# Kernel tuning notes

Hardware: AMD Instinct MI355X
Metric: run time of the kernel (lower is better)

Reference implementation:

```python
import jax, jax.numpy as jnp
import numpy as np

N = 40000
E = 640000
IN_CH = 256
HEADS = 4
C = 32  # hidden_channels per head
NEG_SLOPE = 0.2  # PyG GATConv default


def setup_inputs() -> dict:
    key = jax.random.key(0)
    k1, k2, k3, k4, k5, k6 = jax.random.split(key, 6)
    x = jax.random.normal(k1, (N, IN_CH), dtype=jnp.float32)
    edge_index = jax.random.randint(k2, (2, E), 0, N, dtype=jnp.int64)
    batch = jnp.zeros((N,), dtype=jnp.int64)
    # GATConv params (glorot-ish scale)
    W = jax.random.normal(k3, (IN_CH, HEADS * C), dtype=jnp.float32) / np.sqrt(IN_CH)
    att_src = jax.random.normal(k4, (HEADS, C), dtype=jnp.float32) / np.sqrt(C)
    att_dst = jax.random.normal(k5, (HEADS, C), dtype=jnp.float32) / np.sqrt(C)
    bias = jnp.zeros((HEADS * C,), dtype=jnp.float32)
    return {"x": x, "edge_index": edge_index, "batch": batch,
            "W": W, "att_src": att_src, "att_dst": att_dst, "bias": bias}


def _gat_forward(x, src, dst, W, att_src, att_dst, bias):
    n = x.shape[0]
    xp = (x @ W).reshape(n, HEADS, C)                      # [N,H,C]
    a_src = jnp.einsum('nhc,hc->nh', xp, att_src)          # [N,H]
    a_dst = jnp.einsum('nhc,hc->nh', xp, att_dst)          # [N,H]
    e = a_src[src] + a_dst[dst]                            # [E',H]
    e = jnp.where(e > 0, e, NEG_SLOPE * e)                 # LeakyReLU
    # segment softmax over edges grouped by destination node
    e_max = jax.ops.segment_max(e, dst, num_segments=n)    # [N,H]
    e_exp = jnp.exp(e - e_max[dst])                        # [E',H]
    e_sum = jax.ops.segment_sum(e_exp, dst, num_segments=n)
    alpha = e_exp / e_sum[dst]                             # [E',H]
    # (attention dropout p=0.6 is identity in eval mode)
    msgs = alpha[:, :, None] * xp[src]                     # [E',H,C]
    out = jax.ops.segment_sum(msgs, dst, num_segments=n)   # [N,H,C]
    out = out.reshape(n, HEADS * C) + bias                 # concat heads
    return jax.nn.relu(out)


def reference(x, edge_index, batch, W, att_src, att_dst, bias):
    n = x.shape[0]
    loops = jnp.arange(n, dtype=edge_index.dtype)
    src = jnp.concatenate([edge_index[0], loops])          # add self-loops (PyG default)
    dst = jnp.concatenate([edge_index[1], loops])
    return _gat_forward(x, src, dst, W, att_src, att_dst, bias)
```

## Files before the change

### kernel.cpp

```cpp
#include <hip/hip_runtime.h>
#include <hip/hip_bf16.h>
#include <stdint.h>

#define IN_CH 256
#define HC    128
#define HEADS 4
#define CPH   32
#define NEG_SLOPE 0.2f

#define NB3    625
#define BCAP3  1408
#define EPB    4096

using f32x4  = __attribute__((ext_vector_type(4))) float;
using bf16x8 = __attribute__((ext_vector_type(8))) short;
using f16x8  = __attribute__((ext_vector_type(8))) _Float16;

__global__ __launch_bounds__(256) void k_prep(const float* __restrict__ W,
                                              unsigned short* __restrict__ wpk,
                                              int* __restrict__ bcur) {
    const int t = threadIdx.x, s = blockIdx.x;
    if (s == 0) for (int i = t; i < NB3; i += 256) bcur[i] = 0;
    __shared__ float Wl[32][128];
#pragma unroll
    for (int j = 0; j < 4; ++j) {
        int idx4 = t + j * 256;
        int kk = idx4 >> 5, c4 = (idx4 & 31) * 4;
        *(float4*)(&Wl[kk][c4]) = *(const float4*)(W + (size_t)(s * 32 + kk) * HC + c4);
    }
    __syncthreads();
#pragma unroll
    for (int j = 0; j < 4; ++j) {
        int o = t + j * 256;
        int lane = o & 63, hilo = (o >> 6) & 1, ct = o >> 7;
        const int kk0 = (lane >> 4) * 8;
        const int col = ct * 16 + (lane & 15);
        unsigned short tmp[8];
#pragma unroll
        for (int e = 0; e < 8; ++e) {
            float f = Wl[kk0 + e][col];
            unsigned int u = __float_as_uint(f);
            if (hilo == 0) {
                tmp[e] = (unsigned short)(u >> 16);
            } else {
                float fl = f - __uint_as_float(u & 0xFFFF0000u);
                tmp[e] = (unsigned short)(__float_as_uint(fl) >> 16);
            }
        }
        uint4 ov;
        ov.x = tmp[0] | ((unsigned int)tmp[1] << 16);
        ov.y = tmp[2] | ((unsigned int)tmp[3] << 16);
        ov.z = tmp[4] | ((unsigned int)tmp[5] << 16);
        ov.w = tmp[6] | ((unsigned int)tmp[7] << 16);
        ((uint4*)wpk)[s * 1024 + o] = ov;
    }
}

__device__ inline void cvt_hilo(const float4& a, const float4& b, bf16x8& hi, bf16x8& lo) {
    const float f[8] = {a.x, a.y, a.z, a.w, b.x, b.y, b.z, b.w};
#pragma unroll
    for (int e = 0; e < 8; ++e) {
        unsigned int u = __float_as_uint(f[e]);
        hi[e] = (short)(u >> 16);
        float fl = f[e] - __uint_as_float(u & 0xFFFF0000u);
        lo[e] = (short)(__float_as_uint(fl) >> 16);
    }
}

__global__ __launch_bounds__(256) void k_work(const float* __restrict__ x,
                                              const unsigned short* __restrict__ wpk,
                                              const float* __restrict__ att_src,
                                              const float* __restrict__ att_dst,
                                              unsigned short* __restrict__ xp,
                                              float* __restrict__ asrc,
                                              float* __restrict__ adst,
                                              const int* __restrict__ ei,
                                              int* __restrict__ bcur,
                                              unsigned int* __restrict__ ebuf,
                                              int E, int n, int nbin) {
    if (blockIdx.x < (unsigned)nbin) {
        __shared__ int hist[NB3], base[NB3];
        const int t = threadIdx.x;
        const int e0 = blockIdx.x * EPB;
        const int EN = E + n;
        for (int i = t; i < NB3; i += 256) hist[i] = 0;
        __syncthreads();

        unsigned int pk[16];
        int rk[16];
#pragma unroll
        for (int j = 0; j < 16; ++j) {
            int e = e0 + j * 256 + t;
            if (e < EN) {
                int s, d;
                if (e < E) { s = ei[e]; d = ei[E + e]; } else { s = d = e - E; }
                pk[j] = ((unsigned int)d << 16) | (unsigned int)s;
                rk[j] = atomicAdd(&hist[d >> 6], 1);
            } else {
                pk[j] = 0xFFFFFFFFu;
                rk[j] = 0;
            }
        }
        __syncthreads();
        for (int i = t; i < NB3; i += 256) {
            int c = hist[i];
            base[i] = c ? atomicAdd(&bcur[i], c) : 0;
        }
        __syncthreads();
#pragma unroll
        for (int j = 0; j < 16; ++j) {
            if (pk[j] != 0xFFFFFFFFu) {
                int b = pk[j] >> 22;
                int pos = base[b] + rk[j];
                if (pos < BCAP3)
                    ebuf[(size_t)b * BCAP3 + pos] = pk[j];
            }
        }
        return;
    }

    const int wv = (blockIdx.x - nbin) * 4 + (threadIdx.x >> 6);
    const int m0 = (wv >> 1) * 16;
    const int h2 = wv & 1;
    if (m0 >= n) return;
    const int l  = threadIdx.x & 63;
    const int lr = l & 15;
    const int q  = l >> 4;
    const int kq = q * 8;

    f32x4 acc[4];
    const f32x4 zero = {0.f, 0.f, 0.f, 0.f};
#pragma unroll
    for (int j = 0; j < 4; ++j) acc[j] = zero;

    const int arow_idx = (m0 + lr < n) ? (m0 + lr) : (n - 1);
    const float* arow = x + (size_t)arow_idx * IN_CH + kq;
    const uint4* wb = (const uint4*)wpk + l;
    const int ctb = h2 * 4;

    float4 aLb[2], aHb[2];
    aLb[0] = *(const float4*)(arow);
    aHb[0] = *(const float4*)(arow + 4);

    uint4 sbh[2][2], sbl[2][2];
#pragma unroll
    for (int j = 0; j < 2; ++j) {
        sbh[0][j] = wb[((ctb + j) * 2 + 0) * 64];
        sbl[0][j] = wb[((ctb + j) * 2 + 1) * 64];
    }

#pragma unroll
    for (int s = 0; s < 8; ++s) {
        const int kc = s * 32;
        const int p = s & 1, pn = p ^ 1;
#pragma unroll
        for (int j = 0; j < 2; ++j) {
            sbh[1][j] = wb[((s * 8 + ctb + 2 + j) * 2 + 0) * 64];
            sbl[1][j] = wb[((s * 8 + ctb + 2 + j) * 2 + 1) * 64];
        }
        bf16x8 ahi, alo;
        cvt_hilo(aLb[p], aHb[p], ahi, alo);
#pragma unroll
        for (int j = 0; j < 2; ++j) {
            bf16x8 bhi = __builtin_bit_cast(bf16x8, sbh[0][j]);
            bf16x8 blo = __builtin_bit_cast(bf16x8, sbl[0][j]);
            acc[j] = __builtin_amdgcn_mfma_f32_16x16x32_bf16(alo, bhi, acc[j], 0, 0, 0);
            acc[j] = __builtin_amdgcn_mfma_f32_16x16x32_bf16(ahi, blo, acc[j], 0, 0, 0);
            acc[j] = __builtin_amdgcn_mfma_f32_16x16x32_bf16(ahi, bhi, acc[j], 0, 0, 0);
        }
        if (s < 7) {
#pragma unroll
            for (int j = 0; j < 2; ++j) {
                sbh[0][j] = wb[(((s + 1) * 8 + ctb + j) * 2 + 0) * 64];
                sbl[0][j] = wb[(((s + 1) * 8 + ctb + j) * 2 + 1) * 64];
            }
            aLb[pn] = *(const float4*)(arow + kc + 32);
            aHb[pn] = *(const float4*)(arow + kc + 36);
        }
#pragma unroll
        for (int j = 0; j < 2; ++j) {
            bf16x8 bhi = __builtin_bit_cast(bf16x8, sbh[1][j]);
            bf16x8 blo = __builtin_bit_cast(bf16x8, sbl[1][j]);
            acc[2 + j] = __builtin_amdgcn_mfma_f32_16x16x32_bf16(alo, bhi, acc[2 + j], 0, 0, 0);
            acc[2 + j] = __builtin_amdgcn_mfma_f32_16x16x32_bf16(ahi, blo, acc[2 + j], 0, 0, 0);
            acc[2 + j] = __builtin_amdgcn_mfma_f32_16x16x32_bf16(ahi, bhi, acc[2 + j], 0, 0, 0);
        }
    }

    float as_c[4], ad_c[4];
#pragma unroll
    for (int j = 0; j < 4; ++j) {
        as_c[j] = att_src[(ctb + j) * 16 + lr];
        ad_c[j] = att_dst[(ctb + j) * 16 + lr];
    }
#pragma unroll
    for (int hp = 0; hp < 2; ++hp)
#pragma unroll
        for (int r = 0; r < 4; ++r) {
            float s = acc[2 * hp][r] * as_c[2 * hp] + acc[2 * hp + 1][r] * as_c[2 * hp + 1];
            float d = acc[2 * hp][r] * ad_c[2 * hp] + acc[2 * hp + 1][r] * ad_c[2 * hp + 1];
            s += __shfl_xor(s, 1, 64); s += __shfl_xor(s, 2, 64);
            s += __shfl_xor(s, 4, 64); s += __shfl_xor(s, 8, 64);
            d += __shfl_xor(d, 1, 64); d += __shfl_xor(d, 2, 64);
            d += __shfl_xor(d, 4, 64); d += __shfl_xor(d, 8, 64);
            if (lr == 0) {
                int row = m0 + q * 4 + r;
                if (row < n) {
                    asrc[(size_t)row * 4 + h2 * 2 + hp] = s;
                    adst[(size_t)row * 4 + h2 * 2 + hp] = d;
                }
            }
        }

#pragma unroll
    for (int r = 0; r < 4; ++r) {
        int row = m0 + q * 4 + r;
        if (row < n) {
            unsigned short* xr = xp + (size_t)row * HC + h2 * 64 + lr;
#pragma unroll
            for (int j = 0; j < 4; ++j) {
                _Float16 hv = (_Float16)acc[j][r];
                xr[j * 16] = __builtin_bit_cast(unsigned short, hv);
            }
        }
    }
}

__global__ __launch_bounds__(512) void k_fgat(const int* __restrict__ bcur,
                                              const unsigned int* __restrict__ ebuf,
                                              const float* __restrict__ asrc,
                                              const float* __restrict__ adst,
                                              const unsigned short* __restrict__ xp,
                                              const float* __restrict__ bias,
                                              float* __restrict__ out, int n) {
    __shared__ unsigned short sL[BCAP3];
    __shared__ int lcnt[64];
    __shared__ int loff[65];
    const int b = blockIdx.x, t = threadIdx.x;
    const int m = min(bcur[b], BCAP3);
    const unsigned int* eb = ebuf + (size_t)b * BCAP3;

    unsigned int pk[3];
#pragma unroll
    for (int j = 0; j < 3; ++j) {
        int i = t + j * 512;
        pk[j] = (i < m) ? eb[i] : 0xFFFFFFFFu;
    }
    if (t < 64) lcnt[t] = 0;
    __syncthreads();
    int rk[3];
#pragma unroll
    for (int j = 0; j < 3; ++j)
        if (pk[j] != 0xFFFFFFFFu)
            rk[j] = atomicAdd(&lcnt[(pk[j] >> 16) & 63], 1);
    __syncthreads();
    if (t < 64) {
        int v = lcnt[t];
        int sum = v;
#pragma unroll
        for (int off = 1; off < 64; off <<= 1) {
            int u = __shfl_up(sum, off, 64);
            if (t >= off) sum += u;
        }
        loff[t] = sum - v;
        if (t == 63) loff[64] = sum;
    }
    __syncthreads();
#pragma unroll
    for (int j = 0; j < 3; ++j)
        if (pk[j] != 0xFFFFFFFFu) {
            int ln = (pk[j] >> 16) & 63;
            sL[loff[ln] + rk[j]] = (unsigned short)(pk[j] & 0xFFFFu);
        }
    __syncthreads();

    const int lane = t & 63;
    const int cl = lane & 15;
    const int eg = lane >> 4;
    const int hh = cl >> 2;
    const float4* bp = (const float4*)bias + cl * 2;
    const float4 b0 = bp[0], b1 = bp[1];

#pragma unroll
    for (int i8 = 0; i8 < 8; ++i8) {
        const int ln = (t >> 6) * 8 + i8;
        const int nd = b * 64 + ln;
        if (nd >= n) continue;
        const int s0 = loff[ln], e0 = loff[ln + 1];
        const float ad2 = adst[(size_t)nd * 4 + hh];

        float4 a0 = make_float4(0.f, 0.f, 0.f, 0.f);
        float4 a1 = make_float4(0.f, 0.f, 0.f, 0.f);
        float Z = 0.f;

        int i = s0;
        for (; i + 8 <= e0; i += 8) {
            int sa = sL[i + eg];
            int sb = sL[i + 4 + eg];
            float ta = asrc[(size_t)sa * 4 + hh] + ad2;
            float tb = asrc[(size_t)sb * 4 + hh] + ad2;
            uint4 ua = *(const uint4*)(xp + (size_t)sa * HC + cl * 8);
            uint4 ub = *(const uint4*)(xp + (size_t)sb * HC + cl * 8);
            f16x8 va = __builtin_bit_cast(f16x8, ua);
            f16x8 vb = __builtin_bit_cast(f16x8, ub);
            ta = ta > 0.f ? ta : NEG_SLOPE * ta;
            tb = tb > 0.f ? tb : NEG_SLOPE * tb;
            float pa = __expf(ta);
            float pb = __expf(tb);
            Z += pa + pb;
            a0.x += pa * (float)va[0]; a0.y += pa * (float)va[1];
            a0.z += pa * (float)va[2]; a0.w += pa * (float)va[3];
            a1.x += pa * (float)va[4]; a1.y += pa * (float)va[5];
            a1.z += pa * (float)va[6]; a1.w += pa * (float)va[7];
            a0.x += pb * (float)vb[0]; a0.y += pb * (float)vb[1];
            a0.z += pb * (float)vb[2]; a0.w += pb * (float)vb[3];
            a1.x += pb * (float)vb[4]; a1.y += pb * (float)vb[5];
            a1.z += pb * (float)vb[6]; a1.w += pb * (float)vb[7];
        }
        for (; i < e0; i += 4) {
            if (i + eg < e0) {
                int s = sL[i + eg];
                float tt = asrc[(size_t)s * 4 + hh] + ad2;
                uint4 u = *(const uint4*)(xp + (size_t)s * HC + cl * 8);
                f16x8 v = __builtin_bit_cast(f16x8, u);
                tt = tt > 0.f ? tt : NEG_SLOPE * tt;
                float p = __expf(tt);
                Z += p;
                a0.x += p * (float)v[0]; a0.y += p * (float)v[1];
                a0.z += p * (float)v[2]; a0.w += p * (float)v[3];
                a1.x += p * (float)v[4]; a1.y += p * (float)v[5];
                a1.z += p * (float)v[6]; a1.w += p * (float)v[7];
            }
        }

#pragma unroll
        for (int off = 16; off < 64; off <<= 1) {
            a0.x += __shfl_xor(a0.x, off, 64); a0.y += __shfl_xor(a0.y, off, 64);
            a0.z += __shfl_xor(a0.z, off, 64); a0.w += __shfl_xor(a0.w, off, 64);
            a1.x += __shfl_xor(a1.x, off, 64); a1.y += __shfl_xor(a1.y, off, 64);
            a1.z += __shfl_xor(a1.z, off, 64); a1.w += __shfl_xor(a1.w, off, 64);
            Z += __shfl_xor(Z, off, 64);
        }

        if (eg == 0) {
            const float rZ = 1.0f / Z;
            float4 o0, o1;
            o0.x = fmaxf(a0.x * rZ + b0.x, 0.f); o0.y = fmaxf(a0.y * rZ + b0.y, 0.f);
            o0.z = fmaxf(a0.z * rZ + b0.z, 0.f); o0.w = fmaxf(a0.w * rZ + b0.w, 0.f);
            o1.x = fmaxf(a1.x * rZ + b1.x, 0.f); o1.y = fmaxf(a1.y * rZ + b1.y, 0.f);
            o1.z = fmaxf(a1.z * rZ + b1.z, 0.f); o1.w = fmaxf(a1.w * rZ + b1.w, 0.f);
            float4* op = (float4*)(out + (size_t)nd * HC) + cl * 2;
            op[0] = o0; op[1] = o1;
        }
    }
}

extern "C" void kernel_launch(void* const* d_in, const int* in_sizes, int n_in,
                              void* d_out, int out_size, void* d_ws, size_t ws_size,
                              hipStream_t stream) {
    const float* x       = (const float*)d_in[0];
    const int*   ei      = (const int*)d_in[1];
    const float* W       = (const float*)d_in[3];
    const float* att_src = (const float*)d_in[4];
    const float* att_dst = (const float*)d_in[5];
    const float* bias    = (const float*)d_in[6];
    float* out = (float*)d_out;

    const int n = in_sizes[0] / IN_CH;
    const int E = in_sizes[1] / 2;
    const int EN = E + n;
    const int nbin = (EN + EPB - 1) / EPB;
    const int ngemm = (((n + 15) / 16) * 2 + 3) / 4;
    const int nbkt = (n + 63) / 64;

    unsigned short* xp = (unsigned short*)d_ws;
    float* asrc = (float*)(xp + (size_t)n * HC);
    float* adst = asrc + (size_t)n * HEADS;
    int*   bcur  = (int*)(adst + (size_t)n * HEADS);
    unsigned int* ebuf = (unsigned int*)(bcur + NB3);
    unsigned short* wpk = (unsigned short*)(((uintptr_t)(ebuf + (size_t)NB3 * BCAP3) + 63) & ~(uintptr_t)63);

    k_prep<<<8, 256, 0, stream>>>(W, wpk, bcur);
    k_work<<<nbin + ngemm, 256, 0, stream>>>(x, wpk, att_src, att_dst,
                                             xp, asrc, adst, ei, bcur, ebuf,
                                             E, n, nbin);
    k_fgat<<<nbkt, 512, 0, stream>>>(bcur, ebuf, asrc, adst, xp, bias, out, n);
}
```

Before: 71.32 us.

## Stage 16-row x tile in LDS and split GEMM heads across four waves

The GEMM part of k_work now uses one block per 16-row tile. The block cooperatively loads the x rows into padded shared memory, and each of its four waves computes one head (32 columns). Before, each wave handled two heads and read its x rows straight from global memory, so the same x data was read twice by separate waves. The change removes that duplicate global read and lowers per-wave register use, at the cost of a block barrier, LDS traffic, and twice as many GEMM blocks. It also drops the A-operand double-buffering, so global-load latency is now exposed at the tile load.

```diff
diff --git a/kernel.cpp b/kernel.cpp
--- a/kernel.cpp
+++ b/kernel.cpp
@@ -11,6 +11,7 @@
 #define NB3    625
 #define BCAP3  1408
 #define EPB    4096
+#define ALDP   260
 
 using f32x4  = __attribute__((ext_vector_type(4))) float;
 using bf16x8 = __attribute__((ext_vector_type(8))) short;
@@ -78,8 +79,11 @@
                                               int* __restrict__ bcur,
                                               unsigned int* __restrict__ ebuf,
                                               int E, int n, int nbin) {
+    __shared__ __align__(16) char smem[16 * ALDP * 4];
+
     if (blockIdx.x < (unsigned)nbin) {
-        __shared__ int hist[NB3], base[NB3];
+        int* hist = (int*)smem;
+        int* base = hist + NB3;
         const int t = threadIdx.x;
         const int e0 = blockIdx.x * EPB;
         const int EN = E + n;
@@ -119,109 +123,97 @@
         return;
     }
 
-    const int wv = (blockIdx.x - nbin) * 4 + (threadIdx.x >> 6);
-    const int m0 = (wv >> 1) * 16;
-    const int h2 = wv & 1;
+    const int bg = blockIdx.x - nbin;
+    const int m0 = bg * 16;
     if (m0 >= n) return;
-    const int l  = threadIdx.x & 63;
-    const int lr = l & 15;
-    const int q  = l >> 4;
-    const int kq = q * 8;
-
-    f32x4 acc[4];
+    const int tid = threadIdx.x;
+    const int wvl = tid >> 6;
+    const int l   = tid & 63;
+    const int lr  = l & 15;
+    const int q   = l >> 4;
+    const int kq  = q * 8;
+
+    float (*xls)[ALDP] = (float(*)[ALDP])smem;
+    {
+        const float* xb = x + (size_t)m0 * IN_CH;
+#pragma unroll
+        for (int j = 0; j < 4; ++j) {
+            int idx = tid + j * 256;
+            int row = idx >> 6, k4 = (idx & 63) * 4;
+            float4 v = *(const float4*)(xb + (size_t)row * IN_CH + k4);
+            *(float4*)(&xls[row][k4]) = v;
+        }
+    }
+    __syncthreads();
+
+    f32x4 acc[2];
     const f32x4 zero = {0.f, 0.f, 0.f, 0.f};
-#pragma unroll
-    for (int j = 0; j < 4; ++j) acc[j] = zero;
-
-    const int arow_idx = (m0 + lr < n) ? (m0 + lr) : (n - 1);
-    const float* arow = x + (size_t)arow_idx * IN_CH + kq;
+    acc[0] = zero; acc[1] = zero;
+
     const uint4* wb = (const uint4*)wpk + l;
-    const int ctb = h2 * 4;
-
-    float4 aLb[2], aHb[2];
-    aLb[0] = *(const float4*)(arow);
-    aHb[0] = *(const float4*)(arow + 4);
-
-    uint4 sbh[2][2], sbl[2][2];
-#pragma unroll
-    for (int j = 0; j < 2; ++j) {
-        sbh[0][j] = wb[((ctb + j) * 2 + 0) * 64];
-        sbl[0][j] = wb[((ctb + j) * 2 + 1) * 64];
-    }
+    const int ctb = wvl * 2;
+
+    uint4 bh0 = wb[((ctb + 0) * 2 + 0) * 64];
+    uint4 bl0 = wb[((ctb + 0) * 2 + 1) * 64];
+    uint4 bh1 = wb[((ctb + 1) * 2 + 0) * 64];
+    uint4 bl1 = wb[((ctb + 1) * 2 + 1) * 64];
 
 #pragma unroll
     for (int s = 0; s < 8; ++s) {
-        const int kc = s * 32;
-        const int p = s & 1, pn = p ^ 1;
-#pragma unroll
-        for (int j = 0; j < 2; ++j) {
-            sbh[1][j] = wb[((s * 8 + ctb + 2 + j) * 2 + 0) * 64];
-            sbl[1][j] = wb[((s * 8 + ctb + 2 + j) * 2 + 1) * 64];
-        }
+        uint4 nh0, nl0, nh1, nl1;
+        if (s < 7) {
+            nh0 = wb[(((s + 1) * 8 + ctb + 0) * 2 + 0) * 64];
+            nl0 = wb[(((s + 1) * 8 + ctb + 0) * 2 + 1) * 64];
+            nh1 = wb[(((s + 1) * 8 + ctb + 1) * 2 + 0) * 64];
+            nl1 = wb[(((s + 1) * 8 + ctb + 1) * 2 + 1) * 64];
+        }
+        float4 aL = *(const float4*)(&xls[lr][s * 32 + kq]);
+        float4 aH = *(const float4*)(&xls[lr][s * 32 + kq + 4]);
         bf16x8 ahi, alo;
-        cvt_hilo(aLb[p], aHb[p], ahi, alo);
-#pragma unroll
-        for (int j = 0; j < 2; ++j) {
-            bf16x8 bhi = __builtin_bit_cast(bf16x8, sbh[0][j]);
-            bf16x8 blo = __builtin_bit_cast(bf16x8, sbl[0][j]);
-            acc[j] = __builtin_amdgcn_mfma_f32_16x16x32_bf16(alo, bhi, acc[j], 0, 0, 0);
-            acc[j] = __builtin_amdgcn_mfma_f32_16x16x32_bf16(ahi, blo, acc[j], 0, 0, 0);
-            acc[j] = __builtin_amdgcn_mfma_f32_16x16x32_bf16(ahi, bhi, acc[j], 0, 0, 0);
-        }
-        if (s < 7) {
-#pragma unroll
-            for (int j = 0; j < 2; ++j) {
-                sbh[0][j] = wb[(((s + 1) * 8 + ctb + j) * 2 + 0) * 64];
-                sbl[0][j] = wb[(((s + 1) * 8 + ctb + j) * 2 + 1) * 64];
-            }
-            aLb[pn] = *(const float4*)(arow + kc + 32);
-            aHb[pn] = *(const float4*)(arow + kc + 36);
-        }
-#pragma unroll
-        for (int j = 0; j < 2; ++j) {
-            bf16x8 bhi = __builtin_bit_cast(bf16x8, sbh[1][j]);
-            bf16x8 blo = __builtin_bit_cast(bf16x8, sbl[1][j]);
-            acc[2 + j] = __builtin_amdgcn_mfma_f32_16x16x32_bf16(alo, bhi, acc[2 + j], 0, 0, 0);
-            acc[2 + j] = __builtin_amdgcn_mfma_f32_16x16x32_bf16(ahi, blo, acc[2 + j], 0, 0, 0);
-            acc[2 + j] = __builtin_amdgcn_mfma_f32_16x16x32_bf16(ahi, bhi, acc[2 + j], 0, 0, 0);
-        }
-    }
-
-    float as_c[4], ad_c[4];
-#pragma unroll
-    for (int j = 0; j < 4; ++j) {
-        as_c[j] = att_src[(ctb + j) * 16 + lr];
-        ad_c[j] = att_dst[(ctb + j) * 16 + lr];
-    }
-#pragma unroll
-    for (int hp = 0; hp < 2; ++hp)
-#pragma unroll
-        for (int r = 0; r < 4; ++r) {
-            float s = acc[2 * hp][r] * as_c[2 * hp] + acc[2 * hp + 1][r] * as_c[2 * hp + 1];
-            float d = acc[2 * hp][r] * ad_c[2 * hp] + acc[2 * hp + 1][r] * ad_c[2 * hp + 1];
-            s += __shfl_xor(s, 1, 64); s += __shfl_xor(s, 2, 64);
-            s += __shfl_xor(s, 4, 64); s += __shfl_xor(s, 8, 64);
-            d += __shfl_xor(d, 1, 64); d += __shfl_xor(d, 2, 64);
-            d += __shfl_xor(d, 4, 64); d += __shfl_xor(d, 8, 64);
-            if (lr == 0) {
-                int row = m0 + q * 4 + r;
-                if (row < n) {
-                    asrc[(size_t)row * 4 + h2 * 2 + hp] = s;
-                    adst[(size_t)row * 4 + h2 * 2 + hp] = d;
-                }
-            }
-        }
+        cvt_hilo(aL, aH, ahi, alo);
+        {
+            bf16x8 h0 = __builtin_bit_cast(bf16x8, bh0);
+            bf16x8 l0 = __builtin_bit_cast(bf16x8, bl0);
+            acc[0] = __builtin_amdgcn_mfma_f32_16x16x32_bf16(alo, h0, acc[0], 0, 0, 0);
+            acc[0] = __builtin_amdgcn_mfma_f32_16x16x32_bf16(ahi, l0, acc[0], 0, 0, 0);
+            acc[0] = __builtin_amdgcn_mfma_f32_16x16x32_bf16(ahi, h0, acc[0], 0, 0, 0);
+            bf16x8 h1 = __builtin_bit_cast(bf16x8, bh1);
+            bf16x8 l1 = __builtin_bit_cast(bf16x8, bl1);
+            acc[1] = __builtin_amdgcn_mfma_f32_16x16x32_bf16(alo, h1, acc[1], 0, 0, 0);
+            acc[1] = __builtin_amdgcn_mfma_f32_16x16x32_bf16(ahi, l1, acc[1], 0, 0, 0);
+            acc[1] = __builtin_amdgcn_mfma_f32_16x16x32_bf16(ahi, h1, acc[1], 0, 0, 0);
+        }
+        if (s < 7) { bh0 = nh0; bl0 = nl0; bh1 = nh1; bl1 = nl1; }
+    }
+
+    float as0 = att_src[(ctb + 0) * 16 + lr], as1 = att_src[(ctb + 1) * 16 + lr];
+    float ad0 = att_dst[(ctb + 0) * 16 + lr], ad1 = att_dst[(ctb + 1) * 16 + lr];
+#pragma unroll
+    for (int r = 0; r < 4; ++r) {
+        float s = acc[0][r] * as0 + acc[1][r] * as1;
+        float d = acc[0][r] * ad0 + acc[1][r] * ad1;
+        s += __shfl_xor(s, 1, 64); s += __shfl_xor(s, 2, 64);
+        s += __shfl_xor(s, 4, 64); s += __shfl_xor(s, 8, 64);
+        d += __shfl_xor(d, 1, 64); d += __shfl_xor(d, 2, 64);
+        d += __shfl_xor(d, 4, 64); d += __shfl_xor(d, 8, 64);
+        if (lr == 0) {
+            int row = m0 + q * 4 + r;
+            if (row < n) {
+                asrc[(size_t)row * 4 + wvl] = s;
+                adst[(size_t)row * 4 + wvl] = d;
+            }
+        }
+    }
 
 #pragma unroll
     for (int r = 0; r < 4; ++r) {
         int row = m0 + q * 4 + r;
         if (row < n) {
-            unsigned short* xr = xp + (size_t)row * HC + h2 * 64 + lr;
-#pragma unroll
-            for (int j = 0; j < 4; ++j) {
-                _Float16 hv = (_Float16)acc[j][r];
-                xr[j * 16] = __builtin_bit_cast(unsigned short, hv);
-            }
+            unsigned short* xr = xp + (size_t)row * HC + wvl * 32 + lr;
+            _Float16 h0 = (_Float16)acc[0][r];
+            _Float16 h1 = (_Float16)acc[1][r];
+            xr[0]  = __builtin_bit_cast(unsigned short, h0);
+            xr[16] = __builtin_bit_cast(unsigned short, h1);
         }
     }
 }
@@ -370,7 +362,7 @@
     const int E = in_sizes[1] / 2;
     const int EN = E + n;
     const int nbin = (EN + EPB - 1) / EPB;
-    const int ngemm = (((n + 15) / 16) * 2 + 3) / 4;
+    const int ngemm = (n + 15) / 16;
     const int nbkt = (n + 63) / 64;
 
     unsigned short* xp = (unsigned short*)d_ws;
```

Result: faster. 64.93 us (-9.0%).
